# Performance work log

Measured on AMD Instinct MI355X. Metric: run time of the kernel, lower is better.

The kernel has to match this reference:

```python
import jax, jax.numpy as jnp
import numpy as np

B = 32        # decoding requests
S = 2048      # max kv length per request (pool slots per request)
H = 32        # query heads
HKV = 8       # kv heads (GQA group = 4)
D = 128       # head dim
SCALE = 0.08838834764831845  # 1/sqrt(D)
NEG = -1e30


def setup_inputs() -> dict:
    key = jax.random.key(0)
    ks = jax.random.split(key, 6)
    q = jax.random.normal(ks[0], (B, H * D), jnp.float32)
    k = jax.random.normal(ks[1], (B, HKV * D), jnp.float32)
    v = jax.random.normal(ks[2], (B, HKV * D), jnp.float32)
    key_buffer = jax.random.normal(ks[3], (B * S, HKV, D), jnp.float32)
    value_buffer = jax.random.normal(ks[4], (B * S, HKV, D), jnp.float32)
    # request b owns contiguous pool slots [b*S, (b+1)*S)
    req_to_token = jnp.arange(B * S, dtype=jnp.int32).reshape(B, S)
    # seq_lens includes the new decode token
    seq_lens = jax.random.randint(ks[5], (B,), S // 2, S + 1, dtype=jnp.int32)
    # new token is written at the last occupied slot of each request
    out_cache_loc = jnp.arange(B, dtype=jnp.int32) * S + seq_lens - 1
    return {"q": q, "k": k, "v": v,
            "key_buffer": key_buffer, "value_buffer": value_buffer,
            "req_to_token": req_to_token, "seq_lens": seq_lens,
            "out_cache_loc": out_cache_loc}


def reference(q, k, v, key_buffer, value_buffer, req_to_token, seq_lens, out_cache_loc):
    # store_kv_cache: write new token's K/V into the paged pool
    k3 = k.reshape(B, HKV, D)
    v3 = v.reshape(B, HKV, D)
    kb = key_buffer.at[out_cache_loc].set(k3)
    vb = value_buffer.at[out_cache_loc].set(v3)
    # token attention: gather KV via page table, masked softmax attention
    K = kb[req_to_token]   # [B, S, HKV, D]
    V = vb[req_to_token]   # [B, S, HKV, D]
    qg = (q * SCALE).reshape(B, HKV, H // HKV, D)      # GQA grouping [B, HKV, G, D]
    scores = jnp.einsum('bkgd,bskd->bkgs', qg, K)      # [B, HKV, G, S]
    valid = jnp.arange(S, dtype=jnp.int32)[None, :] < seq_lens[:, None]  # [B, S]
    scores = jnp.where(valid[:, None, None, :], scores, NEG)
    p = jax.nn.softmax(scores, axis=-1)
    o = jnp.einsum('bkgs,bskd->bkgd', p, V)            # [B, HKV, G, D]
    return o.reshape(B, H * D)
```

## Files before the change

### kernel.cpp

```cpp
#include <hip/hip_runtime.h>

#define BB 32
#define SS 2048
#define HH 32
#define HKV 8
#define GG 4
#define DD 128
#define SCALE 0.08838834764831845f
#define NEG -1e30f
#define NSPLIT 8
#define CHUNK (SS / NSPLIT)
#define NWAVES 4
#define PARTIAL_STRIDE 520

__global__ __launch_bounds__(256, 8) void attn_partial(
    const float* __restrict__ q,
    const float* __restrict__ k,
    const float* __restrict__ v,
    const float* __restrict__ key_buffer,
    const float* __restrict__ value_buffer,
    const int* __restrict__ req_to_token,
    const int* __restrict__ seq_lens,
    const int* __restrict__ out_cache_loc,
    float* __restrict__ partials)
{
    const int bid   = blockIdx.x;
    const int b     = bid / (HKV * NSPLIT);
    const int rem   = bid % (HKV * NSPLIT);
    const int h     = rem / NSPLIT;
    const int split = rem % NSPLIT;
    const int tid   = threadIdx.x;
    const int wave  = tid >> 6;
    const int lane  = tid & 63;

    __shared__ float q_lds[GG * DD];
    __shared__ float o_lds[NWAVES][GG][DD];
    __shared__ float l_lds[NWAVES][GG];
    __shared__ float pv_lds[NWAVES][64][GG];
    __shared__ int   tok_lds[NWAVES][64];

    const int seq_len = seq_lens[b];
    const int loc     = out_cache_loc[b];

    {
        const float* qb = q + ((size_t)b * HH + h * GG) * DD;
        q_lds[tid]       = qb[tid] * SCALE;
        q_lds[tid + 256] = qb[tid + 256] * SCALE;
    }
    __syncthreads();

    const int start = split * CHUNK;
    const int end_  = min(start + CHUNK, seq_len);
    float* pbase = partials + (size_t)bid * PARTIAL_STRIDE;

    if (start >= end_) {
        pbase[tid]       = 0.0f;
        pbase[tid + 256] = 0.0f;
        if (tid < GG) pbase[516 + tid] = 0.0f;
        return;
    }

    const int* rt = req_to_token + (size_t)b * SS;
    const float4* q4  = (const float4*)q_lds;
    const float4* kbh = (const float4*)key_buffer   + h * (DD / 4);
    const float4* vbh = (const float4*)value_buffer + h * (DD / 4);
    const float4* kfresh = (const float4*)(k + ((size_t)b * HKV + h) * DD);
    const float4* vfresh = (const float4*)(v + ((size_t)b * HKV + h) * DD);

    const int pos   = start + wave * 64 + lane;
    const bool valid = pos < end_;
    const int pp    = valid ? pos : end_ - 1;
    const int tok   = rt[pp];
    const float4* krow = (pp == seq_len - 1)
        ? kfresh : (kbh + (size_t)tok * (HKV * DD / 4));

    float sc[GG] = {0.f, 0.f, 0.f, 0.f};
    #pragma unroll 8
    for (int d4 = 0; d4 < DD / 4; ++d4) {
        float4 kv = krow[d4];
        #pragma unroll
        for (int g = 0; g < GG; ++g) {
            float4 qv = q4[g * (DD / 4) + d4];
            sc[g] += kv.x * qv.x + kv.y * qv.y + kv.z * qv.z + kv.w * qv.w;
        }
    }
    if (!valid) { sc[0] = NEG; sc[1] = NEG; sc[2] = NEG; sc[3] = NEG; }

    float4 ev = make_float4(__expf(sc[0]), __expf(sc[1]),
                            __expf(sc[2]), __expf(sc[3]));
    *(float4*)&pv_lds[wave][lane][0] = ev;
    tok_lds[wave][lane] = tok;

    const int hp = lane >> 5;
    const int dq = lane & 31;
    float acc[GG][4];
    float lsum[GG] = {0.f, 0.f, 0.f, 0.f};
    #pragma unroll
    for (int g = 0; g < GG; ++g)
        acc[g][0] = acc[g][1] = acc[g][2] = acc[g][3] = 0.f;

    const int nvalid = min(end_ - (start + wave * 64), 64);
    if (nvalid > 0) {
        const int npairs = (nvalid + 1) >> 1;
        #pragma unroll 8
        for (int j = 0; j < npairs; ++j) {
            int    i     = 2 * j + hp;
            float4 pw    = *(const float4*)&pv_lds[wave][i][0];
            int    tok_s = tok_lds[wave][i];
            const float4* vrow = (tok_s == loc)
                ? vfresh : (vbh + (size_t)tok_s * (HKV * DD / 4));
            float4 vv = vrow[dq];
            acc[0][0] += pw.x * vv.x; acc[0][1] += pw.x * vv.y;
            acc[0][2] += pw.x * vv.z; acc[0][3] += pw.x * vv.w;
            acc[1][0] += pw.y * vv.x; acc[1][1] += pw.y * vv.y;
            acc[1][2] += pw.y * vv.z; acc[1][3] += pw.y * vv.w;
            acc[2][0] += pw.z * vv.x; acc[2][1] += pw.z * vv.y;
            acc[2][2] += pw.z * vv.z; acc[2][3] += pw.z * vv.w;
            acc[3][0] += pw.w * vv.x; acc[3][1] += pw.w * vv.y;
            acc[3][2] += pw.w * vv.z; acc[3][3] += pw.w * vv.w;
            lsum[0] += pw.x; lsum[1] += pw.y;
            lsum[2] += pw.z; lsum[3] += pw.w;
        }
    }

    #pragma unroll
    for (int g = 0; g < GG; ++g) {
        #pragma unroll
        for (int c = 0; c < 4; ++c)
            acc[g][c] += __shfl_xor(acc[g][c], 32);
        lsum[g] += __shfl_xor(lsum[g], 32);
    }

    if (lane < 32) {
        #pragma unroll
        for (int g = 0; g < GG; ++g)
            ((float4*)o_lds[wave][g])[dq] =
                make_float4(acc[g][0], acc[g][1], acc[g][2], acc[g][3]);
    }
    if (lane == 0) {
        #pragma unroll
        for (int g = 0; g < GG; ++g) l_lds[wave][g] = lsum[g];
    }
    __syncthreads();

    {
        int g  = tid >> 6;
        int d0 = (tid & 63) * 2;
        float den = l_lds[0][g] + l_lds[1][g] + l_lds[2][g] + l_lds[3][g];
        float o0 = o_lds[0][g][d0]     + o_lds[1][g][d0]
                 + o_lds[2][g][d0]     + o_lds[3][g][d0];
        float o1 = o_lds[0][g][d0 + 1] + o_lds[1][g][d0 + 1]
                 + o_lds[2][g][d0 + 1] + o_lds[3][g][d0 + 1];
        pbase[g * DD + d0]     = o0;
        pbase[g * DD + d0 + 1] = o1;
        if ((tid & 63) == 0) pbase[516 + g] = den;
    }
}

__global__ __launch_bounds__(128) void attn_combine(
    const float* __restrict__ partials, float* __restrict__ out)
{
    const int bh = blockIdx.x;
    const int d  = threadIdx.x;
    const int b  = bh / HKV;
    const int h  = bh % HKV;
    const float* pb = partials + (size_t)bh * NSPLIT * PARTIAL_STRIDE;

    #pragma unroll
    for (int g = 0; g < GG; ++g) {
        float den = 0.f, num = 0.f;
        #pragma unroll
        for (int s = 0; s < NSPLIT; ++s) {
            den += pb[s * PARTIAL_STRIDE + 516 + g];
            num += pb[s * PARTIAL_STRIDE + g * DD + d];
        }
        out[((size_t)b * HH + (h * GG + g)) * DD + d] = num / den;
    }
}

extern "C" void kernel_launch(void* const* d_in, const int* in_sizes, int n_in,
                              void* d_out, int out_size, void* d_ws, size_t ws_size,
                              hipStream_t stream)
{
    const float* q  = (const float*)d_in[0];
    const float* k  = (const float*)d_in[1];
    const float* v  = (const float*)d_in[2];
    const float* key_buffer   = (const float*)d_in[3];
    const float* value_buffer = (const float*)d_in[4];
    const int* req_to_token  = (const int*)d_in[5];
    const int* seq_lens      = (const int*)d_in[6];
    const int* out_cache_loc = (const int*)d_in[7];
    float* out      = (float*)d_out;
    float* partials = (float*)d_ws;

    attn_partial<<<BB * HKV * NSPLIT, 256, 0, stream>>>(
        q, k, v, key_buffer, value_buffer,
        req_to_token, seq_lens, out_cache_loc, partials);
    attn_combine<<<BB * HKV, 128, 0, stream>>>(partials, out);
}
```

Baseline: 513.4 us.

## Process all KV heads per block with token-serial loop and shuffle reductions

Each block now covers one request and a 32-token chunk across all 8 KV heads. For every token, the 256 threads read one contiguous 4 KB K row and V row (one float4 per thread), reduce the QK dot products with butterfly shuffles and accumulate P·V in registers. This replaces the per-head blocks with strided 512-byte row accesses and the LDS staging of probabilities. The cost is a serial per-token dependency chain with several shuffles per token, 64 splits per request, and a larger partials buffer for the combine kernel to read.

```diff
diff --git a/kernel.cpp b/kernel.cpp
--- a/kernel.cpp
+++ b/kernel.cpp
@@ -7,13 +7,11 @@
 #define GG 4
 #define DD 128
 #define SCALE 0.08838834764831845f
-#define NEG -1e30f
-#define NSPLIT 8
+#define NSPLIT 64
 #define CHUNK (SS / NSPLIT)
-#define NWAVES 4
-#define PARTIAL_STRIDE 520
+#define PSTRIDE 4128
 
-__global__ __launch_bounds__(256, 8) void attn_partial(
+__global__ __launch_bounds__(256, 4) void attn_partial(
     const float* __restrict__ q,
     const float* __restrict__ k,
     const float* __restrict__ v,
@@ -25,135 +23,103 @@
     float* __restrict__ partials)
 {
     const int bid   = blockIdx.x;
-    const int b     = bid / (HKV * NSPLIT);
-    const int rem   = bid % (HKV * NSPLIT);
-    const int h     = rem / NSPLIT;
-    const int split = rem % NSPLIT;
+    const int b     = bid / NSPLIT;
+    const int split = bid % NSPLIT;
     const int tid   = threadIdx.x;
-    const int wave  = tid >> 6;
-    const int lane  = tid & 63;
+    const int h     = tid >> 5;
+    const int dq    = tid & 31;
+    const int c     = tid & 3;
 
-    __shared__ float q_lds[GG * DD];
-    __shared__ float o_lds[NWAVES][GG][DD];
-    __shared__ float l_lds[NWAVES][GG];
-    __shared__ float pv_lds[NWAVES][64][GG];
-    __shared__ int   tok_lds[NWAVES][64];
+    __shared__ int tok_lds[CHUNK];
 
     const int seq_len = seq_lens[b];
-    const int loc     = out_cache_loc[b];
-
-    {
-        const float* qb = q + ((size_t)b * HH + h * GG) * DD;
-        q_lds[tid]       = qb[tid] * SCALE;
-        q_lds[tid + 256] = qb[tid + 256] * SCALE;
-    }
-    __syncthreads();
-
-    const int start = split * CHUNK;
-    const int end_  = min(start + CHUNK, seq_len);
-    float* pbase = partials + (size_t)bid * PARTIAL_STRIDE;
+    const int start   = split * CHUNK;
+    const int end_    = min(start + CHUNK, seq_len);
+    float* pbase = partials + (size_t)bid * PSTRIDE;
 
     if (start >= end_) {
-        pbase[tid]       = 0.0f;
-        pbase[tid + 256] = 0.0f;
-        if (tid < GG) pbase[516 + tid] = 0.0f;
+        float4 z = make_float4(0.f, 0.f, 0.f, 0.f);
+        float4* p4 = (float4*)pbase;
+        #pragma unroll
+        for (int j = 0; j < 4; ++j) p4[tid + 256 * j] = z;
+        if (tid < 32) pbase[4096 + tid] = 0.f;
         return;
     }
 
-    const int* rt = req_to_token + (size_t)b * SS;
-    const float4* q4  = (const float4*)q_lds;
-    const float4* kbh = (const float4*)key_buffer   + h * (DD / 4);
-    const float4* vbh = (const float4*)value_buffer + h * (DD / 4);
-    const float4* kfresh = (const float4*)(k + ((size_t)b * HKV + h) * DD);
-    const float4* vfresh = (const float4*)(v + ((size_t)b * HKV + h) * DD);
+    if (tid < CHUNK) tok_lds[tid] = req_to_token[(size_t)b * SS + start + tid];
+    __syncthreads();
 
-    const int pos   = start + wave * 64 + lane;
-    const bool valid = pos < end_;
-    const int pp    = valid ? pos : end_ - 1;
-    const int tok   = rt[pp];
-    const float4* krow = (pp == seq_len - 1)
-        ? kfresh : (kbh + (size_t)tok * (HKV * DD / 4));
-
-    float sc[GG] = {0.f, 0.f, 0.f, 0.f};
-    #pragma unroll 8
-    for (int d4 = 0; d4 < DD / 4; ++d4) {
-        float4 kv = krow[d4];
-        #pragma unroll
-        for (int g = 0; g < GG; ++g) {
-            float4 qv = q4[g * (DD / 4) + d4];
-            sc[g] += kv.x * qv.x + kv.y * qv.y + kv.z * qv.z + kv.w * qv.w;
-        }
-    }
-    if (!valid) { sc[0] = NEG; sc[1] = NEG; sc[2] = NEG; sc[3] = NEG; }
-
-    float4 ev = make_float4(__expf(sc[0]), __expf(sc[1]),
-                            __expf(sc[2]), __expf(sc[3]));
-    *(float4*)&pv_lds[wave][lane][0] = ev;
-    tok_lds[wave][lane] = tok;
-
-    const int hp = lane >> 5;
-    const int dq = lane & 31;
-    float acc[GG][4];
-    float lsum[GG] = {0.f, 0.f, 0.f, 0.f};
+    const float4* q4 = (const float4*)q;
+    float4 q4r[GG];
     #pragma unroll
-    for (int g = 0; g < GG; ++g)
-        acc[g][0] = acc[g][1] = acc[g][2] = acc[g][3] = 0.f;
-
-    const int nvalid = min(end_ - (start + wave * 64), 64);
-    if (nvalid > 0) {
-        const int npairs = (nvalid + 1) >> 1;
-        #pragma unroll 8
-        for (int j = 0; j < npairs; ++j) {
-            int    i     = 2 * j + hp;
-            float4 pw    = *(const float4*)&pv_lds[wave][i][0];
-            int    tok_s = tok_lds[wave][i];
-            const float4* vrow = (tok_s == loc)
-                ? vfresh : (vbh + (size_t)tok_s * (HKV * DD / 4));
-            float4 vv = vrow[dq];
-            acc[0][0] += pw.x * vv.x; acc[0][1] += pw.x * vv.y;
-            acc[0][2] += pw.x * vv.z; acc[0][3] += pw.x * vv.w;
-            acc[1][0] += pw.y * vv.x; acc[1][1] += pw.y * vv.y;
-            acc[1][2] += pw.y * vv.z; acc[1][3] += pw.y * vv.w;
-            acc[2][0] += pw.z * vv.x; acc[2][1] += pw.z * vv.y;
-            acc[2][2] += pw.z * vv.z; acc[2][3] += pw.z * vv.w;
-            acc[3][0] += pw.w * vv.x; acc[3][1] += pw.w * vv.y;
-            acc[3][2] += pw.w * vv.z; acc[3][3] += pw.w * vv.w;
-            lsum[0] += pw.x; lsum[1] += pw.y;
-            lsum[2] += pw.z; lsum[3] += pw.w;
-        }
+    for (int g = 0; g < GG; ++g) {
+        float4 t = q4[((size_t)b * HH + h * GG + g) * (DD / 4) + dq];
+        q4r[g] = make_float4(t.x * SCALE, t.y * SCALE, t.z * SCALE, t.w * SCALE);
     }
 
+    const float4* kb4 = (const float4*)key_buffer;
+    const float4* vb4 = (const float4*)value_buffer;
+    const float4* kf4 = (const float4*)k + (size_t)b * (HKV * DD / 4);
+    const float4* vf4 = (const float4*)v + (size_t)b * (HKV * DD / 4);
+
+    float4 accj[4];
+    float  lj[4] = {0.f, 0.f, 0.f, 0.f};
     #pragma unroll
-    for (int g = 0; g < GG; ++g) {
-        #pragma unroll
-        for (int c = 0; c < 4; ++c)
-            acc[g][c] += __shfl_xor(acc[g][c], 32);
-        lsum[g] += __shfl_xor(lsum[g], 32);
+    for (int j = 0; j < 4; ++j) accj[j] = make_float4(0.f, 0.f, 0.f, 0.f);
+
+    const int ntok = end_ - start;
+    for (int t = 0; t < ntok; ++t) {
+        const int  pos  = start + t;
+        const int  tok  = tok_lds[t];
+        const bool last = (pos == seq_len - 1);
+        const float4* ksrc = last ? kf4 : (kb4 + (size_t)tok * (HKV * DD / 4));
+        const float4* vsrc = last ? vf4 : (vb4 + (size_t)tok * (HKV * DD / 4));
+        float4 kv = ksrc[tid];
+        float4 vv = vsrc[tid];
+
+        float v0 = kv.x * q4r[0].x + kv.y * q4r[0].y + kv.z * q4r[0].z + kv.w * q4r[0].w;
+        float v1 = kv.x * q4r[1].x + kv.y * q4r[1].y + kv.z * q4r[1].z + kv.w * q4r[1].w;
+        float v2 = kv.x * q4r[2].x + kv.y * q4r[2].y + kv.z * q4r[2].z + kv.w * q4r[2].w;
+        float v3 = kv.x * q4r[3].x + kv.y * q4r[3].y + kv.z * q4r[3].z + kv.w * q4r[3].w;
+
+        float keepA = (c & 1) ? v1 : v0;
+        float sendA = (c & 1) ? v0 : v1;
+        float a01 = keepA + __shfl_xor(sendA, 1);
+        float keepB = (c & 1) ? v3 : v2;
+        float sendB = (c & 1) ? v2 : v3;
+        float a23 = keepB + __shfl_xor(sendB, 1);
+        float keepC = (c & 2) ? a23 : a01;
+        float sendC = (c & 2) ? a01 : a23;
+        float s = keepC + __shfl_xor(sendC, 2);
+        s += __shfl_xor(s, 4);
+        s += __shfl_xor(s, 8);
+        s += __shfl_xor(s, 16);
+
+        float pw0 = __expf(s);
+        float pw1 = __shfl_xor(pw0, 1);
+        float pw2 = __shfl_xor(pw0, 2);
+        float pw3 = __shfl_xor(pw0, 3);
+
+        accj[0].x += pw0 * vv.x; accj[0].y += pw0 * vv.y;
+        accj[0].z += pw0 * vv.z; accj[0].w += pw0 * vv.w;
+        accj[1].x += pw1 * vv.x; accj[1].y += pw1 * vv.y;
+        accj[1].z += pw1 * vv.z; accj[1].w += pw1 * vv.w;
+        accj[2].x += pw2 * vv.x; accj[2].y += pw2 * vv.y;
+        accj[2].z += pw2 * vv.z; accj[2].w += pw2 * vv.w;
+        accj[3].x += pw3 * vv.x; accj[3].y += pw3 * vv.y;
+        accj[3].z += pw3 * vv.z; accj[3].w += pw3 * vv.w;
+        lj[0] += pw0; lj[1] += pw1; lj[2] += pw2; lj[3] += pw3;
     }
 
-    if (lane < 32) {
+    float4* o4 = (float4*)pbase;
+    #pragma unroll
+    for (int j = 0; j < 4; ++j) {
+        int g = c ^ j;
+        o4[(h * GG + g) * (DD / 4) + dq] = accj[j];
+    }
+    if (dq == 0) {
         #pragma unroll
-        for (int g = 0; g < GG; ++g)
-            ((float4*)o_lds[wave][g])[dq] =
-                make_float4(acc[g][0], acc[g][1], acc[g][2], acc[g][3]);
-    }
-    if (lane == 0) {
-        #pragma unroll
-        for (int g = 0; g < GG; ++g) l_lds[wave][g] = lsum[g];
-    }
-    __syncthreads();
-
-    {
-        int g  = tid >> 6;
-        int d0 = (tid & 63) * 2;
-        float den = l_lds[0][g] + l_lds[1][g] + l_lds[2][g] + l_lds[3][g];
-        float o0 = o_lds[0][g][d0]     + o_lds[1][g][d0]
-                 + o_lds[2][g][d0]     + o_lds[3][g][d0];
-        float o1 = o_lds[0][g][d0 + 1] + o_lds[1][g][d0 + 1]
-                 + o_lds[2][g][d0 + 1] + o_lds[3][g][d0 + 1];
-        pbase[g * DD + d0]     = o0;
-        pbase[g * DD + d0 + 1] = o1;
-        if ((tid & 63) == 0) pbase[516 + g] = den;
+        for (int j = 0; j < 4; ++j) pbase[4096 + h * GG + j] = lj[j];
     }
 }
 
@@ -162,20 +128,17 @@
 {
     const int bh = blockIdx.x;
     const int d  = threadIdx.x;
-    const int b  = bh / HKV;
-    const int h  = bh % HKV;
-    const float* pb = partials + (size_t)bh * NSPLIT * PARTIAL_STRIDE;
+    const int b  = bh / HH;
+    const int qh = bh % HH;
+    const float* pb = partials + (size_t)b * NSPLIT * PSTRIDE;
 
-    #pragma unroll
-    for (int g = 0; g < GG; ++g) {
-        float den = 0.f, num = 0.f;
-        #pragma unroll
-        for (int s = 0; s < NSPLIT; ++s) {
-            den += pb[s * PARTIAL_STRIDE + 516 + g];
-            num += pb[s * PARTIAL_STRIDE + g * DD + d];
-        }
-        out[((size_t)b * HH + (h * GG + g)) * DD + d] = num / den;
+    float num = 0.f, den = 0.f;
+    #pragma unroll 8
+    for (int s = 0; s < NSPLIT; ++s) {
+        num += pb[(size_t)s * PSTRIDE + qh * DD + d];
+        den += pb[(size_t)s * PSTRIDE + 4096 + qh];
     }
+    out[(size_t)b * (HH * DD) + qh * DD + d] = num / den;
 }
 
 extern "C" void kernel_launch(void* const* d_in, const int* in_sizes, int n_in,
@@ -193,8 +156,8 @@
     float* out      = (float*)d_out;
     float* partials = (float*)d_ws;
 
-    attn_partial<<<BB * HKV * NSPLIT, 256, 0, stream>>>(
+    attn_partial<<<BB * NSPLIT, 256, 0, stream>>>(
         q, k, v, key_buffer, value_buffer,
         req_to_token, seq_lens, out_cache_loc, partials);
-    attn_combine<<<BB * HKV, 128, 0, stream>>>(partials, out);
+    attn_combine<<<BB * HH, 128, 0, stream>>>(partials, out);
 }
```

Result: no change. 519.5 us (+1.2%).
